# Kernel optimization log

Measured on AMD Instinct MI355X. Metric: run time of the kernel, lower is better.

The kernel has to match this reference:

```python
import jax, jax.numpy as jnp
import numpy as np

EMBED_DIM = 1024
NUM_HEADS = 16
HEAD_DIM = EMBED_DIM // NUM_HEADS


def setup_inputs() -> dict:
    key = jax.random.key(0)
    ks = jax.random.split(key, 9)
    B, S, D = 2, 2048, EMBED_DIM
    scale = 1.0 / np.sqrt(D)
    x = jax.random.normal(ks[0], (B, S, D), dtype=jnp.float32)
    # nn.Linear weights are [out, in]; store as [in, out] for x @ W
    Wq = jax.random.uniform(ks[1], (D, D), jnp.float32, -scale, scale)
    bq = jax.random.uniform(ks[2], (D,), jnp.float32, -scale, scale)
    Wk = jax.random.uniform(ks[3], (D, D), jnp.float32, -scale, scale)
    bk = jax.random.uniform(ks[4], (D,), jnp.float32, -scale, scale)
    Wv = jax.random.uniform(ks[5], (D, D), jnp.float32, -scale, scale)
    bv = jax.random.uniform(ks[6], (D,), jnp.float32, -scale, scale)
    Wo = jax.random.uniform(ks[7], (D, D), jnp.float32, -scale, scale)
    bo = jax.random.uniform(ks[8], (D,), jnp.float32, -scale, scale)
    return {"x": x, "Wq": Wq, "bq": bq, "Wk": Wk, "bk": bk,
            "Wv": Wv, "bv": bv, "Wo": Wo, "bo": bo}


def reference(x, Wq, bq, Wk, bk, Wv, bv, Wo, bo):
    B, S, D = x.shape
    H, Dh = NUM_HEADS, HEAD_DIM
    q = (x @ Wq + bq).reshape(B, S, H, Dh).transpose(0, 2, 1, 3)  # [B,H,S,Dh]
    k = (x @ Wk + bk).reshape(B, S, H, Dh).transpose(0, 2, 1, 3)
    v = (x @ Wv + bv).reshape(B, S, H, Dh).transpose(0, 2, 1, 3)
    scores = jnp.einsum('bhqd,bhkd->bhqk', q, k) / jnp.sqrt(jnp.float32(Dh))
    attn = jax.nn.softmax(scores, axis=-1)
    out = jnp.einsum('bhqk,bhkd->bhqd', attn, v)  # [B,H,S,Dh]
    out = out.transpose(0, 2, 1, 3).reshape(B, S, D)
    return out @ Wo + bo
```

## Files before the change

### kernel.cpp

```cpp
#include <hip/hip_runtime.h>
#include <hip/hip_bf16.h>
#include <stdint.h>

using f32x4 = __attribute__((ext_vector_type(4))) float;
using s16x8 = __attribute__((ext_vector_type(8))) short;
using s16x4 = __attribute__((ext_vector_type(4))) short;

__device__ __forceinline__ unsigned short f2bf(float f) {
  union { float f; unsigned int u; } v; v.f = f;
  return (unsigned short)((v.u + 0x7FFFu + ((v.u >> 16) & 1u)) >> 16);
}

__device__ __forceinline__ float exp2_(float x) {
  float r;
  asm("v_exp_f32 %0, %1" : "=v"(r) : "v"(x));
  return r;
}

__device__ __forceinline__ s16x4 pk4(float a, float b, float c, float d) {
  union { unsigned u[2]; s16x4 v; } r;
  asm("v_cvt_pk_bf16_f32 %0, %1, %2" : "=v"(r.u[0]) : "v"(a), "v"(b));
  asm("v_cvt_pk_bf16_f32 %0, %1, %2" : "=v"(r.u[1]) : "v"(c), "v"(d));
  return r.v;
}

__device__ __forceinline__ short pbf(float f) {
  __hip_bfloat16 h = __float2bfloat16(f);
  return *(short*)&h;
}

#define GLD16(gp, lp) __builtin_amdgcn_global_load_lds( \
    (const __attribute__((address_space(1))) unsigned int*)(uintptr_t)(gp), \
    (__attribute__((address_space(3))) unsigned int*)(uintptr_t)(lp), 16, 0, 0)

__device__ __forceinline__ f32x4 mfma32(s16x8 a, s16x8 b, f32x4 c) {
  return __builtin_amdgcn_mfma_f32_16x16x32_bf16(a, b, c, 0, 0, 0);
}

#if __has_builtin(__builtin_amdgcn_mfma_f32_16x16x16bf16_1k)
__device__ __forceinline__ f32x4 mfma16(s16x4 a, s16x4 b, f32x4 c) {
  return __builtin_amdgcn_mfma_f32_16x16x16bf16_1k(a, b, c, 0, 0, 0);
}
#else
__device__ __forceinline__ f32x4 mfma16(s16x4 a, s16x4 b, f32x4 c) {
  f32x4 d;
  asm volatile("v_mfma_f32_16x16x16_bf16 %0, %1, %2, %3"
               : "=v"(d) : "v"(a), "v"(b), "v"(c));
  return d;
}
#endif

__global__ __launch_bounds__(256)
void prep(const float* __restrict__ x,
          const float* __restrict__ Wq, const float* __restrict__ Wk,
          const float* __restrict__ Wv, const float* __restrict__ Wo,
          unsigned short* __restrict__ xb, unsigned short* __restrict__ Wt) {
  __shared__ float tile[64][65];
  int blk = blockIdx.x;
  int tid = threadIdx.x;
  if (blk < 1024) {
    const float4* xi = (const float4*)x;
    ushort4* xo = (ushort4*)xb;
    #pragma unroll
    for (int j = 0; j < 4; ++j) {
      int i = blk * 1024 + j * 256 + tid;
      float4 v = xi[i];
      ushort4 o;
      o.x = f2bf(v.x); o.y = f2bf(v.y); o.z = f2bf(v.z); o.w = f2bf(v.w);
      xo[i] = o;
    }
  } else {
    int wid = blk - 1024;
    int which = wid >> 8, t = wid & 255;
    const float* W = (which == 0) ? Wq : (which == 1) ? Wk : (which == 2) ? Wv : Wo;
    unsigned short* dst = Wt + (size_t)which * 1048576;
    int k0 = (t & 15) * 64, n0 = (t >> 4) * 64;
    int tx = tid & 63, ty = tid >> 6;
    #pragma unroll
    for (int j = 0; j < 64; j += 4)
      tile[ty + j][tx] = W[(size_t)(k0 + ty + j) * 1024 + n0 + tx];
    __syncthreads();
    #pragma unroll
    for (int j = 0; j < 64; j += 4)
      dst[(size_t)(n0 + ty + j) * 1024 + k0 + tx] = f2bf(tile[tx][ty + j]);
  }
}

__global__ __launch_bounds__(256)
void qkv_gemm(const unsigned short* __restrict__ A,
              const unsigned short* __restrict__ Bt,
              const float* __restrict__ bq, const float* __restrict__ bk,
              const float* __restrict__ bv,
              unsigned short* __restrict__ qo, unsigned short* __restrict__ kf,
              unsigned short* __restrict__ vf) {
  __shared__ unsigned short ldsA[2][4096];
  __shared__ unsigned short ldsB[2][4096];
  int orig = blockIdx.x;
  int wg = (orig & 7) * 96 + (orig >> 3);
  int bm = wg / 24;
  int bn = wg - bm * 24;
  int m0 = bm << 7, n0 = bn << 7;
  int tid = threadIdx.x;
  int w = tid >> 6, ln = tid & 63;
  int g = ln >> 4, c = ln & 15;
  int wr = w >> 1, wc = w & 1;

  const unsigned short* ga = A + (size_t)(m0 + (tid >> 2)) * 1024 + (tid & 3) * 8;
  const unsigned short* gb = Bt + (size_t)(n0 + (tid >> 2)) * 1024 + (tid & 3) * 8;
  int lb = w * 512;

  f32x4 acc[4][4];
  f32x4 zero = {0.f, 0.f, 0.f, 0.f};
  #pragma unroll
  for (int m = 0; m < 4; ++m)
    #pragma unroll
    for (int n = 0; n < 4; ++n) acc[m][n] = zero;

  GLD16(ga, &ldsA[0][lb]);
  GLD16(ga + 65536, &ldsA[0][2048 + lb]);
  GLD16(gb, &ldsB[0][lb]);
  GLD16(gb + 65536, &ldsB[0][2048 + lb]);
  __syncthreads();

  int aoff = (wr * 64 + c) * 32 + g * 8;
  int boff = (wc * 64 + c) * 32 + g * 8;

  int cur = 0;
  for (int t = 0; t < 32; ++t) {
    if (t < 31) {
      const unsigned short* ga2 = ga + (t + 1) * 32;
      const unsigned short* gb2 = gb + (t + 1) * 32;
      int nb = cur ^ 1;
      GLD16(ga2, &ldsA[nb][lb]);
      GLD16(ga2 + 65536, &ldsA[nb][2048 + lb]);
      GLD16(gb2, &ldsB[nb][lb]);
      GLD16(gb2 + 65536, &ldsB[nb][2048 + lb]);
    }
    s16x8 af[4], bf[4];
    #pragma unroll
    for (int m = 0; m < 4; ++m)
      af[m] = *(const s16x8*)&ldsA[cur][aoff + m * 512];
    #pragma unroll
    for (int n = 0; n < 4; ++n)
      bf[n] = *(const s16x8*)&ldsB[cur][boff + n * 512];
    #pragma unroll
    for (int m = 0; m < 4; ++m)
      #pragma unroll
      for (int n = 0; n < 4; ++n)
        acc[m][n] = mfma32(af[m], bf[n], acc[m][n]);
    __syncthreads();
    cur ^= 1;
  }

  #pragma unroll
  for (int n = 0; n < 4; ++n) {
    int cg = n0 + wc * 64 + n * 16 + c;
    int p = cg >> 10;
    int d = cg & 1023;
    int hh = d >> 6, dh = d & 63;
    const float* bp = (p == 0) ? bq : (p == 1) ? bk : bv;
    float bias = bp[d];
    #pragma unroll
    for (int m = 0; m < 4; ++m) {
      int r = m0 + wr * 64 + m * 16 + g * 4;
      int b = r >> 11, s = r & 2047;
      size_t pv = (size_t)((b << 4) + hh);
      if (p == 2) {
        int T = s >> 4;
        int dtp = dh >> 4;
        ushort4 pk;
        pk.x = f2bf(acc[m][n][0] + bias);
        pk.y = f2bf(acc[m][n][1] + bias);
        pk.z = f2bf(acc[m][n][2] + bias);
        pk.w = f2bf(acc[m][n][3] + bias);
        *(ushort4*)&vf[pv * 131072 + (size_t)((T * 4 + dtp) * 64 + g * 16 + c) * 4] = pk;
      } else if (p == 1) {
        int T = s >> 4;
        int h2 = dh >> 5, gp = (dh >> 3) & 3, j = dh & 7;
        unsigned short* kd = kf + pv * 131072 + T * 1024 + h2 * 512 +
                             (gp * 16 + (s & 15)) * 8 + j;
        kd[0]  = f2bf(acc[m][n][0] + bias);
        kd[8]  = f2bf(acc[m][n][1] + bias);
        kd[16] = f2bf(acc[m][n][2] + bias);
        kd[24] = f2bf(acc[m][n][3] + bias);
      } else {
        const float sc = 0.180336880111120f;
        size_t base = (pv * 2048 + s) * 64 + dh;
        qo[base]       = f2bf((acc[m][n][0] + bias) * sc);
        qo[base + 64]  = f2bf((acc[m][n][1] + bias) * sc);
        qo[base + 128] = f2bf((acc[m][n][2] + bias) * sc);
        qo[base + 192] = f2bf((acc[m][n][3] + bias) * sc);
      }
    }
  }
}

__global__ __launch_bounds__(256, 2)
void attn_fwd(const unsigned short* __restrict__ q,
              const unsigned short* __restrict__ kfb,
              const unsigned short* __restrict__ vfb,
              unsigned short* __restrict__ ao) {
  __shared__ unsigned short ldsKV[2][8192];
  int orig = blockIdx.x;
  int wg = (orig & 7) * 64 + (orig >> 3);
  int pair = wg >> 4, qt = wg & 15;
  int tid = threadIdx.x;
  int w = tid >> 6, ln = tid & 63;
  int g = ln >> 4, c = ln & 15;
  int q0 = qt * 128 + w * 32;
  const unsigned short* qp = q + (size_t)pair * 131072;
  const char* kbase = (const char*)(kfb + (size_t)pair * 131072);
  const char* vbase = (const char*)(vfb + (size_t)pair * 131072);

  const char* ssrc = ((w < 2) ? kbase : vbase) + (w & 1) * 4096;
  int dsto = (w >= 2 ? 8192 : 0) + (w & 1) * 4096;

  s16x8 qf[2][2];
  #pragma unroll
  for (int j = 0; j < 2; ++j)
    #pragma unroll
    for (int h = 0; h < 2; ++h)
      qf[j][h] = *(const s16x8*)&qp[(q0 + j * 16 + c) * 64 + h * 32 + g * 8];

  f32x4 acc[2][4];
  f32x4 zero = {0.f, 0.f, 0.f, 0.f};
  #pragma unroll
  for (int j = 0; j < 2; ++j)
    #pragma unroll
    for (int dt = 0; dt < 4; ++dt) acc[j][dt] = zero;
  float l0 = 0.f, l1 = 0.f;

  #pragma unroll
  for (int j = 0; j < 4; ++j)
    GLD16(ssrc + j * 1024 + ln * 16, (char*)&ldsKV[0][0] + dsto + j * 1024);

  int buf = 0;
  for (int kv0 = 0; kv0 < 2048; kv0 += 64) {
    if (kv0 + 64 < 2048) {
      const char* s2 = ssrc + (kv0 + 64) * 128;
      char* d2 = (char*)&ldsKV[buf ^ 1][0] + dsto;
      #pragma unroll
      for (int j = 0; j < 4; ++j)
        GLD16(s2 + j * 1024 + ln * 16, d2 + j * 1024);
      asm volatile("s_waitcnt vmcnt(4)" ::: "memory");
    } else {
      asm volatile("s_waitcnt vmcnt(0)" ::: "memory");
    }
    __builtin_amdgcn_s_barrier();

    const unsigned short* L = ldsKV[buf];
    s16x8 kc[4][2];
    #pragma unroll
    for (int kt = 0; kt < 4; ++kt) {
      kc[kt][0] = *(const s16x8*)&L[kt * 1024 + ln * 8];
      kc[kt][1] = *(const s16x8*)&L[kt * 1024 + 512 + ln * 8];
    }

    f32x4 st[4][2];
    __builtin_amdgcn_s_setprio(1);
    #pragma unroll
    for (int kt = 0; kt < 4; ++kt)
      #pragma unroll
      for (int j = 0; j < 2; ++j) {
        f32x4 t = zero;
        t = mfma32(kc[kt][0], qf[j][0], t);
        t = mfma32(kc[kt][1], qf[j][1], t);
        st[kt][j] = t;
      }
    __builtin_amdgcn_s_setprio(0);

    s16x4 vv[4][4];
    #pragma unroll
    for (int dt = 0; dt < 4; ++dt)
      #pragma unroll
      for (int kt = 0; kt < 4; ++kt)
        vv[dt][kt] = *(const s16x4*)&L[4096 + kt * 1024 + dt * 256 + ln * 4];

    s16x4 pa[2][4];
    #pragma unroll
    for (int kt = 0; kt < 4; ++kt) {
      float p00 = exp2_(st[kt][0][0]), p01 = exp2_(st[kt][0][1]);
      float p02 = exp2_(st[kt][0][2]), p03 = exp2_(st[kt][0][3]);
      float p10 = exp2_(st[kt][1][0]), p11 = exp2_(st[kt][1][1]);
      float p12 = exp2_(st[kt][1][2]), p13 = exp2_(st[kt][1][3]);
      l0 += (p00 + p01) + (p02 + p03);
      l1 += (p10 + p11) + (p12 + p13);
      pa[0][kt] = pk4(p00, p01, p02, p03);
      pa[1][kt] = pk4(p10, p11, p12, p13);
    }

    __builtin_amdgcn_s_setprio(1);
    #pragma unroll
    for (int dt = 0; dt < 4; ++dt)
      #pragma unroll
      for (int kt = 0; kt < 4; ++kt) {
        acc[0][dt] = mfma16(pa[0][kt], vv[dt][kt], acc[0][dt]);
        acc[1][dt] = mfma16(pa[1][kt], vv[dt][kt], acc[1][dt]);
      }
    __builtin_amdgcn_s_setprio(0);

    __builtin_amdgcn_s_barrier();
    buf ^= 1;
  }

  l0 += __shfl_xor(l0, 16); l0 += __shfl_xor(l0, 32);
  l1 += __shfl_xor(l1, 16); l1 += __shfl_xor(l1, 32);
  float li0 = 1.f / l0, li1 = 1.f / l1;
  int b = pair >> 4, hh = pair & 15;
  #pragma unroll
  for (int e = 0; e < 4; ++e) {
    float i0 = __shfl(li0, g * 4 + e);
    float i1 = __shfl(li1, g * 4 + e);
    size_t r0 = ((size_t)(b * 2048 + q0 + g * 4 + e) * 16 + hh) * 64;
    size_t r1 = ((size_t)(b * 2048 + q0 + 16 + g * 4 + e) * 16 + hh) * 64;
    #pragma unroll
    for (int dt = 0; dt < 4; ++dt) {
      ao[r0 + dt * 16 + c] = (unsigned short)pbf(acc[0][dt][e] * i0);
      ao[r1 + dt * 16 + c] = (unsigned short)pbf(acc[1][dt][e] * i1);
    }
  }
}

__global__ __launch_bounds__(256)
void out_gemm(const unsigned short* __restrict__ A,
              const unsigned short* __restrict__ Bt,
              const float* __restrict__ bo, float* __restrict__ out) {
  __shared__ unsigned short lds[2][6144];
  int orig = blockIdx.x;
  int wg = (orig & 7) * 64 + (orig >> 3);
  int bm = wg >> 3, bn = wg & 7;
  int m0 = bm << 6, n0 = bn << 7;
  int tid = threadIdx.x;
  int w = tid >> 6, ln = tid & 63;
  int g = ln >> 4, c = ln & 15;
  int wr = w >> 1, wc = w & 1;

  const unsigned short* su[3];
  int du[3];
  #pragma unroll
  for (int i = 0; i < 3; ++i) {
    int u = 3 * w + i;
    if (u < 4) {
      su[i] = A + (size_t)(m0 + u * 16 + (ln >> 2)) * 1024 + (ln & 3) * 8;
      du[i] = u * 512;
    } else {
      int v2 = u - 4;
      su[i] = Bt + (size_t)(n0 + v2 * 16 + (ln >> 2)) * 1024 + (ln & 3) * 8;
      du[i] = 2048 + v2 * 512;
    }
  }

  f32x4 acc[2][4];
  f32x4 zero = {0.f, 0.f, 0.f, 0.f};
  #pragma unroll
  for (int m = 0; m < 2; ++m)
    #pragma unroll
    for (int n = 0; n < 4; ++n) acc[m][n] = zero;

  #pragma unroll
  for (int i = 0; i < 3; ++i) GLD16(su[i], &lds[0][du[i]]);
  __syncthreads();

  int aoff = (wr * 32 + c) * 32 + g * 8;
  int boff = 2048 + (wc * 64 + c) * 32 + g * 8;

  int cur = 0;
  for (int t = 0; t < 32; ++t) {
    if (t < 31) {
      int nb = cur ^ 1;
      #pragma unroll
      for (int i = 0; i < 3; ++i) GLD16(su[i] + (t + 1) * 32, &lds[nb][du[i]]);
    }
    s16x8 af[2], bf[4];
    #pragma unroll
    for (int m = 0; m < 2; ++m)
      af[m] = *(const s16x8*)&lds[cur][aoff + m * 512];
    #pragma unroll
    for (int n = 0; n < 4; ++n)
      bf[n] = *(const s16x8*)&lds[cur][boff + n * 512];
    #pragma unroll
    for (int m = 0; m < 2; ++m)
      #pragma unroll
      for (int n = 0; n < 4; ++n)
        acc[m][n] = mfma32(af[m], bf[n], acc[m][n]);
    __syncthreads();
    cur ^= 1;
  }

  #pragma unroll
  for (int n = 0; n < 4; ++n) {
    int cg = n0 + wc * 64 + n * 16 + c;
    float bias = bo[cg];
    #pragma unroll
    for (int m = 0; m < 2; ++m) {
      int r = m0 + wr * 32 + m * 16 + g * 4;
      out[(size_t)r * 1024 + cg] = acc[m][n][0] + bias;
      out[(size_t)(r + 1) * 1024 + cg] = acc[m][n][1] + bias;
      out[(size_t)(r + 2) * 1024 + cg] = acc[m][n][2] + bias;
      out[(size_t)(r + 3) * 1024 + cg] = acc[m][n][3] + bias;
    }
  }
}

extern "C" void kernel_launch(void* const* d_in, const int* in_sizes, int n_in,
                              void* d_out, int out_size, void* d_ws, size_t ws_size,
                              hipStream_t stream) {
  (void)in_sizes; (void)n_in; (void)out_size; (void)ws_size;
  const float* x  = (const float*)d_in[0];
  const float* Wq = (const float*)d_in[1];
  const float* bq = (const float*)d_in[2];
  const float* Wk = (const float*)d_in[3];
  const float* bk = (const float*)d_in[4];
  const float* Wv = (const float*)d_in[5];
  const float* bv = (const float*)d_in[6];
  const float* Wo = (const float*)d_in[7];
  const float* bo = (const float*)d_in[8];
  float* out = (float*)d_out;
  char* ws = (char*)d_ws;
  unsigned short* xb  = (unsigned short*)(ws);
  unsigned short* Wt  = (unsigned short*)(ws + 8388608);
  unsigned short* Wot = (unsigned short*)(ws + 14680064);
  unsigned short* qb  = (unsigned short*)(ws + 16777216);
  unsigned short* kfb = (unsigned short*)(ws + 25165824);
  unsigned short* vfb = (unsigned short*)(ws + 33554432);
  unsigned short* ao  = (unsigned short*)(ws + 41943040);

  prep<<<2048, 256, 0, stream>>>(x, Wq, Wk, Wv, Wo, xb, Wt);
  qkv_gemm<<<768, 256, 0, stream>>>(xb, Wt, bq, bk, bv, qb, kfb, vfb);
  attn_fwd<<<512, 256, 0, stream>>>(qb, kfb, vfb, ao);
  out_gemm<<<512, 256, 0, stream>>>(ao, Wot, bo, out);
}
```

Measured before the change: 109.5 us.

## Double attention query tile per wave and pair V tiles for wider LDS loads

Each attention wave now handles 64 query rows instead of 32, so every K/V tile staged in LDS is reused by twice as many MFMAs, and the grid shrinks from 512 to 256 blocks. The V layout written by the QKV GEMM interleaves pairs of 16-row tiles so the attention kernel can read 8-element vectors and split them into two MFMA operands, halving V LDS read instructions. Score computation is split into two halves interleaved with exp, which limits live score registers. The cost is higher register pressure (launch bounds relaxed to 1 block per SM) and only 256 workgroups, which may underfill the 256 CUs and reduce latency hiding.

```diff
diff --git a/kernel.cpp b/kernel.cpp
--- a/kernel.cpp
+++ b/kernel.cpp
@@ -167,13 +167,15 @@
       size_t pv = (size_t)((b << 4) + hh);
       if (p == 2) {
         int T = s >> 4;
+        int Tp = T >> 1, par = T & 1;
         int dtp = dh >> 4;
         ushort4 pk;
         pk.x = f2bf(acc[m][n][0] + bias);
         pk.y = f2bf(acc[m][n][1] + bias);
         pk.z = f2bf(acc[m][n][2] + bias);
         pk.w = f2bf(acc[m][n][3] + bias);
-        *(ushort4*)&vf[pv * 131072 + (size_t)((T * 4 + dtp) * 64 + g * 16 + c) * 4] = pk;
+        *(ushort4*)&vf[pv * 131072 +
+                       (size_t)(((Tp * 4 + dtp) * 64 + g * 16 + c) * 8 + par * 4)] = pk;
       } else if (p == 1) {
         int T = s >> 4;
         int h2 = dh >> 5, gp = (dh >> 3) & 3, j = dh & 7;
@@ -195,19 +197,19 @@
   }
 }
 
-__global__ __launch_bounds__(256, 2)
+__global__ __launch_bounds__(256, 1)
 void attn_fwd(const unsigned short* __restrict__ q,
               const unsigned short* __restrict__ kfb,
               const unsigned short* __restrict__ vfb,
               unsigned short* __restrict__ ao) {
   __shared__ unsigned short ldsKV[2][8192];
   int orig = blockIdx.x;
-  int wg = (orig & 7) * 64 + (orig >> 3);
-  int pair = wg >> 4, qt = wg & 15;
+  int wg = (orig & 7) * 32 + (orig >> 3);
+  int pair = wg >> 3, qt = wg & 7;
   int tid = threadIdx.x;
   int w = tid >> 6, ln = tid & 63;
   int g = ln >> 4, c = ln & 15;
-  int q0 = qt * 128 + w * 32;
+  int q0 = qt * 256 + w * 64;
   const unsigned short* qp = q + (size_t)pair * 131072;
   const char* kbase = (const char*)(kfb + (size_t)pair * 131072);
   const char* vbase = (const char*)(vfb + (size_t)pair * 131072);
@@ -215,20 +217,20 @@
   const char* ssrc = ((w < 2) ? kbase : vbase) + (w & 1) * 4096;
   int dsto = (w >= 2 ? 8192 : 0) + (w & 1) * 4096;
 
-  s16x8 qf[2][2];
-  #pragma unroll
-  for (int j = 0; j < 2; ++j)
+  s16x8 qf[4][2];
+  #pragma unroll
+  for (int j = 0; j < 4; ++j)
     #pragma unroll
     for (int h = 0; h < 2; ++h)
       qf[j][h] = *(const s16x8*)&qp[(q0 + j * 16 + c) * 64 + h * 32 + g * 8];
 
-  f32x4 acc[2][4];
+  f32x4 acc[4][4];
   f32x4 zero = {0.f, 0.f, 0.f, 0.f};
   #pragma unroll
-  for (int j = 0; j < 2; ++j)
+  for (int j = 0; j < 4; ++j)
     #pragma unroll
     for (int dt = 0; dt < 4; ++dt) acc[j][dt] = zero;
-  float l0 = 0.f, l1 = 0.f;
+  float l[4] = {0.f, 0.f, 0.f, 0.f};
 
   #pragma unroll
   for (int j = 0; j < 4; ++j)
@@ -255,68 +257,76 @@
       kc[kt][0] = *(const s16x8*)&L[kt * 1024 + ln * 8];
       kc[kt][1] = *(const s16x8*)&L[kt * 1024 + 512 + ln * 8];
     }
-
-    f32x4 st[4][2];
+    s16x8 vv2[4][2];
+    #pragma unroll
+    for (int dt = 0; dt < 4; ++dt)
+      #pragma unroll
+      for (int tp = 0; tp < 2; ++tp)
+        vv2[dt][tp] = *(const s16x8*)&L[4096 + tp * 2048 + dt * 512 + ln * 8];
+
+    s16x4 pa[4][4];
+    #pragma unroll
+    for (int ktp = 0; ktp < 2; ++ktp) {
+      f32x4 st[2][4];
+      __builtin_amdgcn_s_setprio(1);
+      #pragma unroll
+      for (int k2 = 0; k2 < 2; ++k2) {
+        int kt = ktp * 2 + k2;
+        #pragma unroll
+        for (int j = 0; j < 4; ++j) {
+          f32x4 t = zero;
+          t = mfma32(kc[kt][0], qf[j][0], t);
+          t = mfma32(kc[kt][1], qf[j][1], t);
+          st[k2][j] = t;
+        }
+      }
+      __builtin_amdgcn_s_setprio(0);
+      #pragma unroll
+      for (int k2 = 0; k2 < 2; ++k2) {
+        int kt = ktp * 2 + k2;
+        #pragma unroll
+        for (int j = 0; j < 4; ++j) {
+          float p0 = exp2_(st[k2][j][0]), p1 = exp2_(st[k2][j][1]);
+          float p2 = exp2_(st[k2][j][2]), p3 = exp2_(st[k2][j][3]);
+          l[j] += (p0 + p1) + (p2 + p3);
+          pa[j][kt] = pk4(p0, p1, p2, p3);
+        }
+      }
+    }
+
     __builtin_amdgcn_s_setprio(1);
     #pragma unroll
-    for (int kt = 0; kt < 4; ++kt)
-      #pragma unroll
-      for (int j = 0; j < 2; ++j) {
-        f32x4 t = zero;
-        t = mfma32(kc[kt][0], qf[j][0], t);
-        t = mfma32(kc[kt][1], qf[j][1], t);
-        st[kt][j] = t;
+    for (int dt = 0; dt < 4; ++dt)
+      #pragma unroll
+      for (int tp = 0; tp < 2; ++tp) {
+        s16x4 vlo = __builtin_shufflevector(vv2[dt][tp], vv2[dt][tp], 0, 1, 2, 3);
+        s16x4 vhi = __builtin_shufflevector(vv2[dt][tp], vv2[dt][tp], 4, 5, 6, 7);
+        #pragma unroll
+        for (int j = 0; j < 4; ++j) {
+          acc[j][dt] = mfma16(pa[j][tp * 2], vlo, acc[j][dt]);
+          acc[j][dt] = mfma16(pa[j][tp * 2 + 1], vhi, acc[j][dt]);
+        }
       }
     __builtin_amdgcn_s_setprio(0);
 
-    s16x4 vv[4][4];
-    #pragma unroll
-    for (int dt = 0; dt < 4; ++dt)
-      #pragma unroll
-      for (int kt = 0; kt < 4; ++kt)
-        vv[dt][kt] = *(const s16x4*)&L[4096 + kt * 1024 + dt * 256 + ln * 4];
-
-    s16x4 pa[2][4];
-    #pragma unroll
-    for (int kt = 0; kt < 4; ++kt) {
-      float p00 = exp2_(st[kt][0][0]), p01 = exp2_(st[kt][0][1]);
-      float p02 = exp2_(st[kt][0][2]), p03 = exp2_(st[kt][0][3]);
-      float p10 = exp2_(st[kt][1][0]), p11 = exp2_(st[kt][1][1]);
-      float p12 = exp2_(st[kt][1][2]), p13 = exp2_(st[kt][1][3]);
-      l0 += (p00 + p01) + (p02 + p03);
-      l1 += (p10 + p11) + (p12 + p13);
-      pa[0][kt] = pk4(p00, p01, p02, p03);
-      pa[1][kt] = pk4(p10, p11, p12, p13);
-    }
-
-    __builtin_amdgcn_s_setprio(1);
-    #pragma unroll
-    for (int dt = 0; dt < 4; ++dt)
-      #pragma unroll
-      for (int kt = 0; kt < 4; ++kt) {
-        acc[0][dt] = mfma16(pa[0][kt], vv[dt][kt], acc[0][dt]);
-        acc[1][dt] = mfma16(pa[1][kt], vv[dt][kt], acc[1][dt]);
-      }
-    __builtin_amdgcn_s_setprio(0);
-
     __builtin_amdgcn_s_barrier();
     buf ^= 1;
   }
 
-  l0 += __shfl_xor(l0, 16); l0 += __shfl_xor(l0, 32);
-  l1 += __shfl_xor(l1, 16); l1 += __shfl_xor(l1, 32);
-  float li0 = 1.f / l0, li1 = 1.f / l1;
   int b = pair >> 4, hh = pair & 15;
   #pragma unroll
-  for (int e = 0; e < 4; ++e) {
-    float i0 = __shfl(li0, g * 4 + e);
-    float i1 = __shfl(li1, g * 4 + e);
-    size_t r0 = ((size_t)(b * 2048 + q0 + g * 4 + e) * 16 + hh) * 64;
-    size_t r1 = ((size_t)(b * 2048 + q0 + 16 + g * 4 + e) * 16 + hh) * 64;
-    #pragma unroll
-    for (int dt = 0; dt < 4; ++dt) {
-      ao[r0 + dt * 16 + c] = (unsigned short)pbf(acc[0][dt][e] * i0);
-      ao[r1 + dt * 16 + c] = (unsigned short)pbf(acc[1][dt][e] * i1);
+  for (int j = 0; j < 4; ++j) {
+    float lj = l[j];
+    lj += __shfl_xor(lj, 16);
+    lj += __shfl_xor(lj, 32);
+    float li = 1.f / lj;
+    #pragma unroll
+    for (int e = 0; e < 4; ++e) {
+      float iv = __shfl(li, g * 4 + e);
+      size_t r0 = ((size_t)(b * 2048 + q0 + j * 16 + g * 4 + e) * 16 + hh) * 64;
+      #pragma unroll
+      for (int dt = 0; dt < 4; ++dt)
+        ao[r0 + dt * 16 + c] = (unsigned short)pbf(acc[j][dt][e] * iv);
     }
   }
 }
@@ -427,6 +437,6 @@
 
   prep<<<2048, 256, 0, stream>>>(x, Wq, Wk, Wv, Wo, xb, Wt);
   qkv_gemm<<<768, 256, 0, stream>>>(xb, Wt, bq, bk, bv, qb, kfb, vfb);
-  attn_fwd<<<512, 256, 0, stream>>>(qb, kfb, vfb, ao);
+  attn_fwd<<<256, 256, 0, stream>>>(qb, kfb, vfb, ao);
   out_gemm<<<512, 256, 0, stream>>>(ao, Wot, bo, out);
 }
```

Result: slower. 117.5 us (+7.4%).

## Software-pipeline attention loop: overlap PV of previous tile with QK of current

Applied to the files above, without the earlier changes.

Restructures the attention inner loop into a software pipeline with a triple-buffered LDS K/V ring. Each iteration issues the QK MFMAs for the current tile, then the PV MFMAs for the previous tile's probabilities, then the exp of the current scores, so the exp work can overlap matrix work. The V fragment layout written by the projection kernel is interleaved in pairs of 16-row tiles, so that PV operands load as 16-byte reads instead of 8-byte ones. This costs 50% more LDS per block, which may reduce occupancy, plus extra registers for two probability buffers.

```diff
diff --git a/kernel.cpp b/kernel.cpp
--- a/kernel.cpp
+++ b/kernel.cpp
@@ -167,13 +167,15 @@
       size_t pv = (size_t)((b << 4) + hh);
       if (p == 2) {
         int T = s >> 4;
+        int Tp = T >> 1, par = T & 1;
         int dtp = dh >> 4;
         ushort4 pk;
         pk.x = f2bf(acc[m][n][0] + bias);
         pk.y = f2bf(acc[m][n][1] + bias);
         pk.z = f2bf(acc[m][n][2] + bias);
         pk.w = f2bf(acc[m][n][3] + bias);
-        *(ushort4*)&vf[pv * 131072 + (size_t)((T * 4 + dtp) * 64 + g * 16 + c) * 4] = pk;
+        *(ushort4*)&vf[pv * 131072 +
+                       (size_t)(((Tp * 4 + dtp) * 64 + g * 16 + c) * 8 + par * 4)] = pk;
       } else if (p == 1) {
         int T = s >> 4;
         int h2 = dh >> 5, gp = (dh >> 3) & 3, j = dh & 7;
@@ -200,7 +202,7 @@
               const unsigned short* __restrict__ kfb,
               const unsigned short* __restrict__ vfb,
               unsigned short* __restrict__ ao) {
-  __shared__ unsigned short ldsKV[2][8192];
+  __shared__ unsigned short ldsKV[3][8192];
   int orig = blockIdx.x;
   int wg = (orig & 7) * 64 + (orig >> 3);
   int pair = wg >> 4, qt = wg & 15;
@@ -234,74 +236,99 @@
   for (int j = 0; j < 4; ++j)
     GLD16(ssrc + j * 1024 + ln * 16, (char*)&ldsKV[0][0] + dsto + j * 1024);
 
-  int buf = 0;
-  for (int kv0 = 0; kv0 < 2048; kv0 += 64) {
-    if (kv0 + 64 < 2048) {
-      const char* s2 = ssrc + (kv0 + 64) * 128;
-      char* d2 = (char*)&ldsKV[buf ^ 1][0] + dsto;
-      #pragma unroll
-      for (int j = 0; j < 4; ++j)
-        GLD16(s2 + j * 1024 + ln * 16, d2 + j * 1024);
-      asm volatile("s_waitcnt vmcnt(4)" ::: "memory");
-    } else {
-      asm volatile("s_waitcnt vmcnt(0)" ::: "memory");
-    }
-    __builtin_amdgcn_s_barrier();
-
-    const unsigned short* L = ldsKV[buf];
-    s16x8 kc[4][2];
-    #pragma unroll
-    for (int kt = 0; kt < 4; ++kt) {
-      kc[kt][0] = *(const s16x8*)&L[kt * 1024 + ln * 8];
-      kc[kt][1] = *(const s16x8*)&L[kt * 1024 + 512 + ln * 8];
-    }
-
-    f32x4 st[4][2];
-    __builtin_amdgcn_s_setprio(1);
-    #pragma unroll
-    for (int kt = 0; kt < 4; ++kt)
+  const unsigned short* L0 = ldsKV[0];
+  const unsigned short* L1 = ldsKV[1];
+  const unsigned short* L2 = ldsKV[2];
+  s16x4 paA[2][4], paB[2][4];
+
+#define ATTN_ITER(T, LC, LP, LN, PAC, PAP)                                     \
+  {                                                                            \
+    if ((T) < 31) {                                                            \
+      const char* s2 = ssrc + ((T) + 1) * 8192;                                \
+      char* d2 = (char*)(LN) + dsto;                                           \
+      _Pragma("unroll")                                                        \
+      for (int j = 0; j < 4; ++j)                                              \
+        GLD16(s2 + j * 1024 + ln * 16, d2 + j * 1024);                         \
+      asm volatile("s_waitcnt vmcnt(4)" ::: "memory");                         \
+    } else {                                                                   \
+      asm volatile("s_waitcnt vmcnt(0)" ::: "memory");                         \
+    }                                                                          \
+    __builtin_amdgcn_s_barrier();                                              \
+                                    \
+    s16x8 kc[4][2];                                                            \
+    _Pragma("unroll")                                                          \
+    for (int kt = 0; kt < 4; ++kt) {                                           \
+      kc[kt][0] = *(const s16x8*)&(LC)[kt * 1024 + ln * 8];                    \
+      kc[kt][1] = *(const s16x8*)&(LC)[kt * 1024 + 512 + ln * 8];              \
+    }                                                                          \
+    f32x4 st[4][2];                                                            \
+    __builtin_amdgcn_s_setprio(1);                                             \
+    _Pragma("unroll")                                                          \
+    for (int kt = 0; kt < 4; ++kt)                                             \
+      _Pragma("unroll")                                                        \
+      for (int j = 0; j < 2; ++j) {                                            \
+        f32x4 t2 = zero;                                                       \
+        t2 = mfma32(kc[kt][0], qf[j][0], t2);                                  \
+        t2 = mfma32(kc[kt][1], qf[j][1], t2);                                  \
+        st[kt][j] = t2;                                                        \
+      }                                                                        \
+    __builtin_amdgcn_s_setprio(0);                                             \
+                 \
+    if ((T) > 0) {                                                             \
+      __builtin_amdgcn_s_setprio(1);                                           \
+      _Pragma("unroll")                                                        \
+      for (int dt = 0; dt < 4; ++dt)                                           \
+        _Pragma("unroll")                                                      \
+        for (int tp = 0; tp < 2; ++tp) {                                       \
+          s16x8 vv = *(const s16x8*)&(LP)[4096 + tp * 2048 + dt * 512 + ln * 8]; \
+          s16x4 vlo = __builtin_shufflevector(vv, vv, 0, 1, 2, 3);             \
+          s16x4 vhi = __builtin_shufflevector(vv, vv, 4, 5, 6, 7);             \
+          _Pragma("unroll")                                                    \
+          for (int j = 0; j < 2; ++j) {                                        \
+            acc[j][dt] = mfma16((PAP)[j][tp * 2], vlo, acc[j][dt]);            \
+            acc[j][dt] = mfma16((PAP)[j][tp * 2 + 1], vhi, acc[j][dt]);        \
+          }                                                                    \
+        }                                                                      \
+      __builtin_amdgcn_s_setprio(0);                                           \
+    }                                                                          \
+                              \
+    _Pragma("unroll")                                                          \
+    for (int kt = 0; kt < 4; ++kt) {                                           \
+      float p00 = exp2_(st[kt][0][0]), p01 = exp2_(st[kt][0][1]);              \
+      float p02 = exp2_(st[kt][0][2]), p03 = exp2_(st[kt][0][3]);              \
+      float p10 = exp2_(st[kt][1][0]), p11 = exp2_(st[kt][1][1]);              \
+      float p12 = exp2_(st[kt][1][2]), p13 = exp2_(st[kt][1][3]);              \
+      l0 += (p00 + p01) + (p02 + p03);                                         \
+      l1 += (p10 + p11) + (p12 + p13);                                         \
+      (PAC)[0][kt] = pk4(p00, p01, p02, p03);                                  \
+      (PAC)[1][kt] = pk4(p10, p11, p12, p13);                                  \
+    }                                                                          \
+    __builtin_amdgcn_s_barrier();                                              \
+  }
+
+  for (int t = 0; t < 32; t += 2) {
+    ATTN_ITER(t,     L0, L2, L1, paA, paB);
+    ATTN_ITER(t + 1, L1, L0, L2, paB, paA);
+    const unsigned short* tmp = L2;
+    L2 = L1; L1 = L0; L0 = tmp;
+  }
+#undef ATTN_ITER
+
+  __builtin_amdgcn_s_setprio(1);
+  #pragma unroll
+  for (int dt = 0; dt < 4; ++dt)
+    #pragma unroll
+    for (int tp = 0; tp < 2; ++tp) {
+      s16x8 vv = *(const s16x8*)&L2[4096 + tp * 2048 + dt * 512 + ln * 8];
+      s16x4 vlo = __builtin_shufflevector(vv, vv, 0, 1, 2, 3);
+      s16x4 vhi = __builtin_shufflevector(vv, vv, 4, 5, 6, 7);
       #pragma unroll
       for (int j = 0; j < 2; ++j) {
-        f32x4 t = zero;
-        t = mfma32(kc[kt][0], qf[j][0], t);
-        t = mfma32(kc[kt][1], qf[j][1], t);
-        st[kt][j] = t;
+        acc[j][dt] = mfma16(paB[j][tp * 2], vlo, acc[j][dt]);
+        acc[j][dt] = mfma16(paB[j][tp * 2 + 1], vhi, acc[j][dt]);
       }
-    __builtin_amdgcn_s_setprio(0);
-
-    s16x4 vv[4][4];
-    #pragma unroll
-    for (int dt = 0; dt < 4; ++dt)
-      #pragma unroll
-      for (int kt = 0; kt < 4; ++kt)
-        vv[dt][kt] = *(const s16x4*)&L[4096 + kt * 1024 + dt * 256 + ln * 4];
-
-    s16x4 pa[2][4];
-    #pragma unroll
-    for (int kt = 0; kt < 4; ++kt) {
-      float p00 = exp2_(st[kt][0][0]), p01 = exp2_(st[kt][0][1]);
-      float p02 = exp2_(st[kt][0][2]), p03 = exp2_(st[kt][0][3]);
-      float p10 = exp2_(st[kt][1][0]), p11 = exp2_(st[kt][1][1]);
-      float p12 = exp2_(st[kt][1][2]), p13 = exp2_(st[kt][1][3]);
-      l0 += (p00 + p01) + (p02 + p03);
-      l1 += (p10 + p11) + (p12 + p13);
-      pa[0][kt] = pk4(p00, p01, p02, p03);
-      pa[1][kt] = pk4(p10, p11, p12, p13);
-    }
-
-    __builtin_amdgcn_s_setprio(1);
-    #pragma unroll
-    for (int dt = 0; dt < 4; ++dt)
-      #pragma unroll
-      for (int kt = 0; kt < 4; ++kt) {
-        acc[0][dt] = mfma16(pa[0][kt], vv[dt][kt], acc[0][dt]);
-        acc[1][dt] = mfma16(pa[1][kt], vv[dt][kt], acc[1][dt]);
-      }
-    __builtin_amdgcn_s_setprio(0);
-
-    __builtin_amdgcn_s_barrier();
-    buf ^= 1;
-  }
+    }
+  __builtin_amdgcn_s_setprio(0);
 
   l0 += __shfl_xor(l0, 16); l0 += __shfl_xor(l0, 32);
   l1 += __shfl_xor(l1, 16); l1 += __shfl_xor(l1, 32);
```

Result: no change. 111.4 us (+1.7%).
